# Optimization experiments

Hardware: AMD Instinct MI355X
Metric: run time of the kernel (lower is better)

Reference implementation:

```python
import jax, jax.numpy as jnp
import numpy as np

N_NODES = 50000
N_EDGES = 800000
IN_FEATS = 256
HIDDEN = 128
OUT_FEATS = 64


def setup_inputs() -> dict:
    key = jax.random.key(0)
    k1, k2, k3, k4, k5 = jax.random.split(key, 5)
    x = jax.random.normal(k1, (N_NODES, IN_FEATS), dtype=jnp.float32)
    src = jax.random.randint(k2, (N_EDGES,), 0, N_NODES, dtype=jnp.int64)
    dst = jax.random.randint(k3, (N_EDGES,), 0, N_NODES, dtype=jnp.int64)
    # Glorot-ish init for linear weights (DGL GraphConv uses xavier_uniform)
    W1 = jax.random.normal(k4, (IN_FEATS, HIDDEN), dtype=jnp.float32) / np.sqrt(IN_FEATS)
    W2 = jax.random.normal(k5, (HIDDEN, OUT_FEATS), dtype=jnp.float32) / np.sqrt(HIDDEN)
    b1 = jnp.zeros((HIDDEN,), dtype=jnp.float32)
    b2 = jnp.zeros((OUT_FEATS,), dtype=jnp.float32)
    return {"x": x, "src": src, "dst": dst, "W1": W1, "b1": b1, "W2": W2, "b2": b2}


def _norms(src, dst, n_nodes):
    ones = jnp.ones(src.shape[0], dtype=jnp.float32)
    deg_out = jax.ops.segment_sum(ones, src, num_segments=n_nodes)
    deg_in = jax.ops.segment_sum(ones, dst, num_segments=n_nodes)
    # DGL clamps zero degrees to 1 to avoid inf
    norm_src = jnp.power(jnp.clip(deg_out, 1.0, None), -0.5)  # [N]
    norm_dst = jnp.power(jnp.clip(deg_in, 1.0, None), -0.5)   # [N]
    return norm_src, norm_dst


def _gcn_layer(h, W, b, src, dst, norm_src, norm_dst, n_nodes):
    # norm='both': D_dst^{-1/2} A D_src^{-1/2} (h W) + b
    # multiply by W first (in_feats >= out_feats -> cheaper aggregation)
    m = (h * norm_src[:, None]) @ W            # [N, out]
    agg = jax.ops.segment_sum(m[src], dst, num_segments=n_nodes)  # [N, out]
    return agg * norm_dst[:, None] + b


def reference(x, src, dst, W1, b1, W2, b2):
    n = x.shape[0]
    norm_src, norm_dst = _norms(src, dst, n)
    h = _gcn_layer(x, W1, b1, src, dst, norm_src, norm_dst, n)
    h = jax.nn.relu(h)
    h = _gcn_layer(h, W2, b2, src, dst, norm_src, norm_dst, n)
    return h
```

## Files before the change

### kernel.cpp

```cpp
#include <hip/hip_runtime.h>

#define N_NODES 50000
#define N_EDGES 800000
#define IN_FEATS 256
#define HIDDEN 128
#define OUT_FEATS 64

#define NCHUNK 64
#define EPC 12500
#define NBH 16384
#define NRH 4
#define NBTH (NRH * NBH)
#define HBLKH (NRH * NCHUNK)
#define NBF 8192
#define NRF 7
#define FBLK (NRF * NCHUNK)
#define ROWBLK ((N_NODES + 63) / 64)

typedef _Float16 f16;
typedef _Float16 f16x8 __attribute__((ext_vector_type(8)));
typedef float f32x4 __attribute__((ext_vector_type(4)));

__global__ __launch_bounds__(256) void wtrans(const float* __restrict__ W1,
                                              const float* __restrict__ W2,
                                              f16* __restrict__ W1T,
                                              f16* __restrict__ W2T) {
  int i = blockIdx.x * 256 + threadIdx.x;
  if (i < 128 * 256) {
    int n = i >> 8, k = i & 255;
    W1T[i] = (f16)W1[k * 128 + n];
  } else {
    int j = i - 128 * 256;
    int n = j >> 7, k = j & 127;
    W2T[j] = (f16)W2[k * 64 + n];
  }
}

__global__ __launch_bounds__(256) void hist_gemm_kernel(
    const int* __restrict__ src, const int* __restrict__ dst,
    unsigned* __restrict__ hist_src, unsigned* __restrict__ hist_dst,
    const f16* __restrict__ W1T, const float* __restrict__ x,
    f16* __restrict__ m1) {
  __shared__ __align__(16) unsigned smem[8192];
  if (blockIdx.x < HBLKH) {
    unsigned* ls = smem;
    unsigned* ld2 = smem + NBH / 4;
    const int r = blockIdx.x % NRH;
    const int c = blockIdx.x / NRH;
    const int lo = r * NBH;
    for (int i = threadIdx.x; i < NBH / 4; i += 256) {
      ls[i] = 0;
      ld2[i] = 0;
    }
    __syncthreads();
    const int4* s4 = (const int4*)(src + c * EPC);
    const int4* d4 = (const int4*)(dst + c * EPC);
    for (int i = threadIdx.x; i < EPC / 4; i += 256) {
      int4 s = s4[i];
      int4 d = d4[i];
      unsigned b;
      b = (unsigned)(s.x - lo); if (b < NBH) atomicAdd(&ls[b >> 2], 1u << ((b & 3) << 3));
      b = (unsigned)(s.y - lo); if (b < NBH) atomicAdd(&ls[b >> 2], 1u << ((b & 3) << 3));
      b = (unsigned)(s.z - lo); if (b < NBH) atomicAdd(&ls[b >> 2], 1u << ((b & 3) << 3));
      b = (unsigned)(s.w - lo); if (b < NBH) atomicAdd(&ls[b >> 2], 1u << ((b & 3) << 3));
      b = (unsigned)(d.x - lo); if (b < NBH) atomicAdd(&ld2[b >> 2], 1u << ((b & 3) << 3));
      b = (unsigned)(d.y - lo); if (b < NBH) atomicAdd(&ld2[b >> 2], 1u << ((b & 3) << 3));
      b = (unsigned)(d.z - lo); if (b < NBH) atomicAdd(&ld2[b >> 2], 1u << ((b & 3) << 3));
      b = (unsigned)(d.w - lo); if (b < NBH) atomicAdd(&ld2[b >> 2], 1u << ((b & 3) << 3));
    }
    __syncthreads();
    unsigned* hs = hist_src + ((long)c * NBTH + lo) / 4;
    unsigned* hd = hist_dst + ((long)c * NBTH + lo) / 4;
    for (int i = threadIdx.x; i < NBH / 4; i += 256) {
      hs[i] = ls[i];
      hd[i] = ld2[i];
    }
  } else {
    char* BsBytes = (char*)smem;
    const int rb = blockIdx.x - HBLKH;
    const int wave = threadIdx.x >> 6;
    const int lane = threadIdx.x & 63;
    const int m = lane & 15;
    const int q = lane >> 4;
    const int row0 = rb * 64 + wave * 16;
    const int ra = min(row0 + m, N_NODES - 1);

    f16x8 a[8];
#pragma unroll
    for (int ki = 0; ki < 8; ++ki) {
      const float* p = x + (long)ra * IN_FEATS + ki * 32 + q * 8;
      float4 u0 = *(const float4*)p;
      float4 u1 = *(const float4*)(p + 4);
      a[ki][0] = (f16)u0.x; a[ki][1] = (f16)u0.y;
      a[ki][2] = (f16)u0.z; a[ki][3] = (f16)u0.w;
      a[ki][4] = (f16)u1.x; a[ki][5] = (f16)u1.y;
      a[ki][6] = (f16)u1.z; a[ki][7] = (f16)u1.w;
    }

    for (int h = 0; h < 2; ++h) {
      const int col0 = h * 64;
#pragma unroll
      for (int idx = threadIdx.x; idx < 64 * 32; idx += 256) {
        int n = idx >> 5;
        int kq = idx & 31;
        f16x8 v = *(const f16x8*)(W1T + (col0 + n) * IN_FEATS + kq * 8);
        unsigned bo = (unsigned)(n * 512 + kq * 16);
        bo ^= (unsigned)((n & 7) << 4);
        *(f16x8*)(BsBytes + bo) = v;
      }
      __syncthreads();

      f32x4 acc[4];
#pragma unroll
      for (int t = 0; t < 4; ++t) acc[t] = (f32x4){0.f, 0.f, 0.f, 0.f};

#pragma unroll
      for (int ki = 0; ki < 8; ++ki) {
        const int kb2 = (ki * 32 + q * 8) * 2;
#pragma unroll
        for (int t = 0; t < 4; ++t) {
          int nrow = t * 16 + m;
          unsigned bo = (unsigned)(nrow * 512 + kb2);
          bo ^= (unsigned)((nrow & 7) << 4);
          f16x8 bfr = *(const f16x8*)(BsBytes + bo);
          acc[t] = __builtin_amdgcn_mfma_f32_16x16x32_f16(a[ki], bfr, acc[t], 0, 0, 0);
        }
      }
      __syncthreads();

#pragma unroll
      for (int rr = 0; rr < 4; ++rr) {
        int row = row0 + q * 4 + rr;
        if (row < N_NODES) {
#pragma unroll
          for (int t = 0; t < 4; ++t)
            m1[(long)row * HIDDEN + col0 + t * 16 + m] = (f16)acc[t][rr];
        }
      }
    }
  }
}

__global__ __launch_bounds__(256) void reduce_kernel(
    const unsigned* __restrict__ hist_src, unsigned* __restrict__ hist_dst,
    int* __restrict__ deg_in, float* __restrict__ norm_src,
    float* __restrict__ norm_dst, int* __restrict__ partial) {
  const unsigned char* hs = (const unsigned char*)hist_src;
  unsigned char* hd = (unsigned char*)hist_dst;
  int n = blockIdx.x * 256 + threadIdx.x;
  int run = 0;
  if (n < N_NODES) {
    int so = 0;
#pragma unroll 8
    for (int c = 0; c < NCHUNK; ++c) so += hs[(long)c * NBTH + n];
    norm_src[n] = rsqrtf((float)max(so, 1));
#pragma unroll 8
    for (int c = 0; c < NCHUNK; ++c) {
      int t = hd[(long)c * NBTH + n];
      hd[(long)c * NBTH + n] = (unsigned char)run;
      run += t;
    }
    deg_in[n] = run;
    norm_dst[n] = rsqrtf((float)max(run, 1));
  }
  __shared__ int sd[256];
  sd[threadIdx.x] = run;
  __syncthreads();
  for (int s = 128; s > 0; s >>= 1) {
    if (threadIdx.x < s) sd[threadIdx.x] += sd[threadIdx.x + s];
    __syncthreads();
  }
  if (threadIdx.x == 0) partial[blockIdx.x] = sd[0];
}

__global__ __launch_bounds__(256) void scan3(const int* __restrict__ deg,
                                             const int* __restrict__ partial,
                                             int* __restrict__ rowptr) {
  __shared__ int sd[256];
  __shared__ int sp[256];
  const int w = blockIdx.x;
  int pv = (threadIdx.x < 196) ? partial[threadIdx.x] : 0;
  sp[threadIdx.x] = pv;
  __syncthreads();
  for (int off = 1; off < 256; off <<= 1) {
    int t = sp[threadIdx.x] +
            ((threadIdx.x >= off) ? sp[threadIdx.x - off] : 0);
    __syncthreads();
    sp[threadIdx.x] = t;
    __syncthreads();
  }
  const int base = (w == 0) ? 0 : sp[w - 1];
  int i = w * 256 + threadIdx.x;
  int v = (i < N_NODES) ? deg[i] : 0;
  sd[threadIdx.x] = v;
  __syncthreads();
  for (int off = 1; off < 256; off <<= 1) {
    int t = sd[threadIdx.x] +
            ((threadIdx.x >= off) ? sd[threadIdx.x - off] : 0);
    __syncthreads();
    sd[threadIdx.x] = t;
    __syncthreads();
  }
  if (i < N_NODES) rowptr[i] = base + sd[threadIdx.x] - v;
  if (w == 0 && threadIdx.x == 0) rowptr[N_NODES] = N_EDGES;
}

__global__ __launch_bounds__(256) void fill_csr(
    const int* __restrict__ src, const int* __restrict__ dst,
    const int* __restrict__ rowptr, const unsigned* __restrict__ pref32,
    int* __restrict__ col) {
  __shared__ int cur[NBF];
  const unsigned char* pref = (const unsigned char*)pref32;
  const int r = blockIdx.x % NRF;
  const int c = blockIdx.x / NRF;
  const int lo = r * NBF;
  for (int i = threadIdx.x; i < NBF; i += 256) {
    int n = lo + i;
    cur[i] = (n < N_NODES) ? rowptr[n] + pref[(long)c * NBTH + n] : 0;
  }
  __syncthreads();
  const int4* s4 = (const int4*)(src + c * EPC);
  const int4* d4 = (const int4*)(dst + c * EPC);
  for (int i = threadIdx.x; i < EPC / 4; i += 256) {
    int4 s = s4[i];
    int4 d = d4[i];
    unsigned b;
    b = (unsigned)(d.x - lo);
    if (b < NBF) col[atomicAdd(&cur[b], 1)] = s.x;
    b = (unsigned)(d.y - lo);
    if (b < NBF) col[atomicAdd(&cur[b], 1)] = s.y;
    b = (unsigned)(d.z - lo);
    if (b < NBF) col[atomicAdd(&cur[b], 1)] = s.z;
    b = (unsigned)(d.w - lo);
    if (b < NBF) col[atomicAdd(&cur[b], 1)] = s.w;
  }
}

template <int K, int NC, int TN, bool FP32IN>
__global__ __launch_bounds__(256) void gemm_mfma(
    const void* __restrict__ Xv, const f16* __restrict__ WT,
    const float* __restrict__ ns, f16* __restrict__ Mout) {
  constexpr int KI = K / 32;
  constexpr int COLBLK = NC / (TN * 16);
  constexpr int KP = K + 8;
  __shared__ f16 Bs[TN * 16 * KP];

  const int cb = blockIdx.x % COLBLK;
  const int rb = blockIdx.x / COLBLK;
  const int col0 = cb * TN * 16;
  const int wave = threadIdx.x >> 6;
  const int lane = threadIdx.x & 63;
  const int m = lane & 15;
  const int q = lane >> 4;
  const int row0 = rb * 64 + wave * 16;

  for (int idx = threadIdx.x; idx < TN * 16 * (K / 8); idx += 256) {
    int n = idx / (K / 8);
    int kk = idx % (K / 8);
    *(f16x8*)(Bs + n * KP + kk * 8) =
        *(const f16x8*)(WT + (long)(col0 + n) * K + kk * 8);
  }
  __syncthreads();

  const int ra = min(row0 + m, N_NODES - 1);
  const float s = FP32IN ? ns[ra] : 0.f;

  f32x4 acc[TN];
#pragma unroll
  for (int t = 0; t < TN; ++t) acc[t] = (f32x4){0.f, 0.f, 0.f, 0.f};

#pragma unroll
  for (int ki = 0; ki < KI; ++ki) {
    const int kb = ki * 32 + q * 8;
    f16x8 a;
    if (FP32IN) {
      const float* X = (const float*)Xv;
      const float* p = X + (long)ra * K + kb;
      float4 u0 = *(const float4*)p;
      float4 u1 = *(const float4*)(p + 4);
      a[0] = (f16)(u0.x * s); a[1] = (f16)(u0.y * s);
      a[2] = (f16)(u0.z * s); a[3] = (f16)(u0.w * s);
      a[4] = (f16)(u1.x * s); a[5] = (f16)(u1.y * s);
      a[6] = (f16)(u1.z * s); a[7] = (f16)(u1.w * s);
    } else {
      const f16* X = (const f16*)Xv;
      a = *(const f16x8*)(X + (long)ra * K + kb);
    }
#pragma unroll
    for (int t = 0; t < TN; ++t) {
      f16x8 b = *(const f16x8*)(Bs + (t * 16 + m) * KP + kb);
      acc[t] = __builtin_amdgcn_mfma_f32_16x16x32_f16(a, b, acc[t], 0, 0, 0);
    }
  }

#pragma unroll
  for (int r = 0; r < 4; ++r) {
    int row = row0 + q * 4 + r;
    if (row < N_NODES) {
#pragma unroll
      for (int t = 0; t < TN; ++t)
        Mout[(long)row * NC + col0 + t * 16 + m] = (f16)acc[t][r];
    }
  }
}

__global__ __launch_bounds__(256) void gather1_kernel(
    const f16* __restrict__ M, const int* __restrict__ rowptr,
    const int* __restrict__ col, const float* __restrict__ nd,
    const float* __restrict__ ns, const float* __restrict__ b,
    f16* __restrict__ out) {
  constexpr int LPR = 16;
  constexpr int EPW = 64 / LPR;
  const int wave = threadIdx.x >> 6;
  const int lane = threadIdx.x & 63;
  const int eg = lane / LPR;
  const int t = lane % LPR;
  const int n = blockIdx.x * 4 + wave;
  if (n >= N_NODES) return;
  const int beg = rowptr[n];
  const int end = rowptr[n + 1];

  float acc[8];
#pragma unroll
  for (int j = 0; j < 8; ++j) acc[j] = 0.f;

  int i = beg + eg;
  for (; i + EPW < end; i += 2 * EPW) {
    int s0 = col[i];
    int s1 = col[i + EPW];
    float n0 = ns[s0];
    float n1 = ns[s1];
    f16x8 v0 = *(const f16x8*)(M + (long)s0 * HIDDEN + t * 8);
    f16x8 v1 = *(const f16x8*)(M + (long)s1 * HIDDEN + t * 8);
#pragma unroll
    for (int j = 0; j < 8; ++j)
      acc[j] += n0 * (float)v0[j] + n1 * (float)v1[j];
  }
  if (i < end) {
    int s0 = col[i];
    float n0 = ns[s0];
    f16x8 v0 = *(const f16x8*)(M + (long)s0 * HIDDEN + t * 8);
#pragma unroll
    for (int j = 0; j < 8; ++j) acc[j] += n0 * (float)v0[j];
  }

#pragma unroll
  for (int m2 = LPR; m2 < 64; m2 <<= 1)
#pragma unroll
    for (int j = 0; j < 8; ++j) acc[j] += __shfl_xor(acc[j], m2, 64);

  if (eg == 0) {
    float s = nd[n];
    float sn = ns[n];
    float4 bb0 = *(const float4*)(b + t * 8);
    float4 bb1 = *(const float4*)(b + t * 8 + 4);
    f16x8 o;
    o[0] = (f16)(fmaxf(acc[0] * s + bb0.x, 0.f) * sn);
    o[1] = (f16)(fmaxf(acc[1] * s + bb0.y, 0.f) * sn);
    o[2] = (f16)(fmaxf(acc[2] * s + bb0.z, 0.f) * sn);
    o[3] = (f16)(fmaxf(acc[3] * s + bb0.w, 0.f) * sn);
    o[4] = (f16)(fmaxf(acc[4] * s + bb1.x, 0.f) * sn);
    o[5] = (f16)(fmaxf(acc[5] * s + bb1.y, 0.f) * sn);
    o[6] = (f16)(fmaxf(acc[6] * s + bb1.z, 0.f) * sn);
    o[7] = (f16)(fmaxf(acc[7] * s + bb1.w, 0.f) * sn);
    *(f16x8*)(out + (long)n * HIDDEN + t * 8) = o;
  }
}

__global__ __launch_bounds__(256) void gather2_kernel(
    const f16* __restrict__ M, const int* __restrict__ rowptr,
    const int* __restrict__ col, const float* __restrict__ nd,
    const float* __restrict__ b, float* __restrict__ out) {
  constexpr int LPR = 8;
  constexpr int EPW = 64 / LPR;
  const int wave = threadIdx.x >> 6;
  const int lane = threadIdx.x & 63;
  const int eg = lane / LPR;
  const int t = lane % LPR;
  const int n = blockIdx.x * 4 + wave;
  if (n >= N_NODES) return;
  const int beg = rowptr[n];
  const int end = rowptr[n + 1];

  float acc[8];
#pragma unroll
  for (int j = 0; j < 8; ++j) acc[j] = 0.f;

  int i = beg + eg;
  for (; i + EPW < end; i += 2 * EPW) {
    int s0 = col[i];
    int s1 = col[i + EPW];
    f16x8 v0 = *(const f16x8*)(M + (long)s0 * OUT_FEATS + t * 8);
    f16x8 v1 = *(const f16x8*)(M + (long)s1 * OUT_FEATS + t * 8);
#pragma unroll
    for (int j = 0; j < 8; ++j) acc[j] += (float)v0[j] + (float)v1[j];
  }
  if (i < end) {
    int s0 = col[i];
    f16x8 v0 = *(const f16x8*)(M + (long)s0 * OUT_FEATS + t * 8);
#pragma unroll
    for (int j = 0; j < 8; ++j) acc[j] += (float)v0[j];
  }

#pragma unroll
  for (int m2 = LPR; m2 < 64; m2 <<= 1)
#pragma unroll
    for (int j = 0; j < 8; ++j) acc[j] += __shfl_xor(acc[j], m2, 64);

  if (eg == 0) {
    float s = nd[n];
    float4 bb0 = *(const float4*)(b + t * 8);
    float4 bb1 = *(const float4*)(b + t * 8 + 4);
    float4 o0, o1;
    o0.x = acc[0] * s + bb0.x;
    o0.y = acc[1] * s + bb0.y;
    o0.z = acc[2] * s + bb0.z;
    o0.w = acc[3] * s + bb0.w;
    o1.x = acc[4] * s + bb1.x;
    o1.y = acc[5] * s + bb1.y;
    o1.z = acc[6] * s + bb1.z;
    o1.w = acc[7] * s + bb1.w;
    *(float4*)(out + (long)n * OUT_FEATS + t * 8) = o0;
    *(float4*)(out + (long)n * OUT_FEATS + t * 8 + 4) = o1;
  }
}

extern "C" void kernel_launch(void* const* d_in, const int* in_sizes, int n_in,
                              void* d_out, int out_size, void* d_ws,
                              size_t ws_size, hipStream_t stream) {
  const float* x = (const float*)d_in[0];
  const int* src = (const int*)d_in[1];
  const int* dst = (const int*)d_in[2];
  const float* W1 = (const float*)d_in[3];
  const float* b1 = (const float*)d_in[4];
  const float* W2 = (const float*)d_in[5];
  const float* b2 = (const float*)d_in[6];
  float* out = (float*)d_out;

  int* wi = (int*)d_ws;
  int* partial = wi;
  int* rowptr = wi + 256;
  int* deg_in = wi + 50260;
  int* col = wi + 100260;
  float* wf = (float*)d_ws + 900260;
  float* norm_src = wf;
  float* norm_dst = wf + 50000;
  f16* fh = (f16*)(wf + 100000);
  f16* W1T = fh;
  f16* W2T = fh + 128 * 256;
  f16* m1 = W2T + 64 * 128;
  f16* h1p = m1 + (long)50048 * 128;
  f16* m2 = h1p + (long)50048 * 128;

  unsigned* hist_src = (unsigned*)h1p;
  unsigned* hist_dst = hist_src + (long)NCHUNK * NBTH / 4;

  const int nb_nodes = (N_NODES + 255) / 256;

  wtrans<<<160, 256, 0, stream>>>(W1, W2, W1T, W2T);
  hist_gemm_kernel<<<HBLKH + ROWBLK, 256, 0, stream>>>(
      src, dst, hist_src, hist_dst, W1T, x, m1);
  reduce_kernel<<<nb_nodes, 256, 0, stream>>>(hist_src, hist_dst, deg_in,
                                              norm_src, norm_dst, partial);
  scan3<<<nb_nodes, 256, 0, stream>>>(deg_in, partial, rowptr);
  fill_csr<<<FBLK, 256, 0, stream>>>(src, dst, rowptr, hist_dst, col);

  gather1_kernel<<<(N_NODES + 3) / 4, 256, 0, stream>>>(m1, rowptr, col,
                                                        norm_dst, norm_src, b1,
                                                        h1p);

  gemm_mfma<HIDDEN, OUT_FEATS, 4, false>
      <<<ROWBLK, 256, 0, stream>>>(h1p, W2T, norm_src, m2);
  gather2_kernel<<<(N_NODES + 3) / 4, 256, 0, stream>>>(m2, rowptr, col,
                                                        norm_dst, b2, out);
}
```

Before: 221.6 us.

## Fuse layer-1 gather with layer-2 GEMM via shared-memory row tile

Layer-1 aggregation and the second GEMM now run in one kernel. Each 256-thread block aggregates 16 nodes into a shared-memory tile, then multiplies that tile by W2T with one 16x16x32 MFMA per wave per k-step and writes m2 directly. This removes the h1p round trip through global memory and one kernel launch. In exchange each wave processes 4 nodes serially, so there are fewer blocks to hide gather latency, and W2T is read straight from global by every block.

```diff
diff --git a/kernel.cpp b/kernel.cpp
--- a/kernel.cpp
+++ b/kernel.cpp
@@ -236,134 +236,88 @@
   }
 }
 
-template <int K, int NC, int TN, bool FP32IN>
-__global__ __launch_bounds__(256) void gemm_mfma(
-    const void* __restrict__ Xv, const f16* __restrict__ WT,
-    const float* __restrict__ ns, f16* __restrict__ Mout) {
-  constexpr int KI = K / 32;
-  constexpr int COLBLK = NC / (TN * 16);
-  constexpr int KP = K + 8;
-  __shared__ f16 Bs[TN * 16 * KP];
-
-  const int cb = blockIdx.x % COLBLK;
-  const int rb = blockIdx.x / COLBLK;
-  const int col0 = cb * TN * 16;
-  const int wave = threadIdx.x >> 6;
-  const int lane = threadIdx.x & 63;
-  const int m = lane & 15;
-  const int q = lane >> 4;
-  const int row0 = rb * 64 + wave * 16;
-
-  for (int idx = threadIdx.x; idx < TN * 16 * (K / 8); idx += 256) {
-    int n = idx / (K / 8);
-    int kk = idx % (K / 8);
-    *(f16x8*)(Bs + n * KP + kk * 8) =
-        *(const f16x8*)(WT + (long)(col0 + n) * K + kk * 8);
-  }
-  __syncthreads();
-
-  const int ra = min(row0 + m, N_NODES - 1);
-  const float s = FP32IN ? ns[ra] : 0.f;
-
-  f32x4 acc[TN];
-#pragma unroll
-  for (int t = 0; t < TN; ++t) acc[t] = (f32x4){0.f, 0.f, 0.f, 0.f};
-
-#pragma unroll
-  for (int ki = 0; ki < KI; ++ki) {
-    const int kb = ki * 32 + q * 8;
-    f16x8 a;
-    if (FP32IN) {
-      const float* X = (const float*)Xv;
-      const float* p = X + (long)ra * K + kb;
-      float4 u0 = *(const float4*)p;
-      float4 u1 = *(const float4*)(p + 4);
-      a[0] = (f16)(u0.x * s); a[1] = (f16)(u0.y * s);
-      a[2] = (f16)(u0.z * s); a[3] = (f16)(u0.w * s);
-      a[4] = (f16)(u1.x * s); a[5] = (f16)(u1.y * s);
-      a[6] = (f16)(u1.z * s); a[7] = (f16)(u1.w * s);
-    } else {
-      const f16* X = (const f16*)Xv;
-      a = *(const f16x8*)(X + (long)ra * K + kb);
-    }
-#pragma unroll
-    for (int t = 0; t < TN; ++t) {
-      f16x8 b = *(const f16x8*)(Bs + (t * 16 + m) * KP + kb);
-      acc[t] = __builtin_amdgcn_mfma_f32_16x16x32_f16(a, b, acc[t], 0, 0, 0);
-    }
-  }
-
-#pragma unroll
-  for (int r = 0; r < 4; ++r) {
-    int row = row0 + q * 4 + r;
-    if (row < N_NODES) {
-#pragma unroll
-      for (int t = 0; t < TN; ++t)
-        Mout[(long)row * NC + col0 + t * 16 + m] = (f16)acc[t][r];
-    }
-  }
-}
-
-__global__ __launch_bounds__(256) void gather1_kernel(
+__global__ __launch_bounds__(256) void gather_gemm2_kernel(
     const f16* __restrict__ M, const int* __restrict__ rowptr,
     const int* __restrict__ col, const float* __restrict__ nd,
     const float* __restrict__ ns, const float* __restrict__ b,
-    f16* __restrict__ out) {
+    const f16* __restrict__ W2T, f16* __restrict__ m2) {
   constexpr int LPR = 16;
   constexpr int EPW = 64 / LPR;
+  constexpr int RS = 136;
+  __shared__ __align__(16) f16 rows[16 * RS];
   const int wave = threadIdx.x >> 6;
   const int lane = threadIdx.x & 63;
   const int eg = lane / LPR;
   const int t = lane % LPR;
-  const int n = blockIdx.x * 4 + wave;
-  if (n >= N_NODES) return;
-  const int beg = rowptr[n];
-  const int end = rowptr[n + 1];
-
-  float acc[8];
-#pragma unroll
-  for (int j = 0; j < 8; ++j) acc[j] = 0.f;
-
-  int i = beg + eg;
-  for (; i + EPW < end; i += 2 * EPW) {
-    int s0 = col[i];
-    int s1 = col[i + EPW];
-    float n0 = ns[s0];
-    float n1 = ns[s1];
-    f16x8 v0 = *(const f16x8*)(M + (long)s0 * HIDDEN + t * 8);
-    f16x8 v1 = *(const f16x8*)(M + (long)s1 * HIDDEN + t * 8);
-#pragma unroll
-    for (int j = 0; j < 8; ++j)
-      acc[j] += n0 * (float)v0[j] + n1 * (float)v1[j];
-  }
-  if (i < end) {
-    int s0 = col[i];
-    float n0 = ns[s0];
-    f16x8 v0 = *(const f16x8*)(M + (long)s0 * HIDDEN + t * 8);
-#pragma unroll
-    for (int j = 0; j < 8; ++j) acc[j] += n0 * (float)v0[j];
-  }
-
-#pragma unroll
-  for (int m2 = LPR; m2 < 64; m2 <<= 1)
-#pragma unroll
-    for (int j = 0; j < 8; ++j) acc[j] += __shfl_xor(acc[j], m2, 64);
-
-  if (eg == 0) {
-    float s = nd[n];
-    float sn = ns[n];
-    float4 bb0 = *(const float4*)(b + t * 8);
-    float4 bb1 = *(const float4*)(b + t * 8 + 4);
-    f16x8 o;
-    o[0] = (f16)(fmaxf(acc[0] * s + bb0.x, 0.f) * sn);
-    o[1] = (f16)(fmaxf(acc[1] * s + bb0.y, 0.f) * sn);
-    o[2] = (f16)(fmaxf(acc[2] * s + bb0.z, 0.f) * sn);
-    o[3] = (f16)(fmaxf(acc[3] * s + bb0.w, 0.f) * sn);
-    o[4] = (f16)(fmaxf(acc[4] * s + bb1.x, 0.f) * sn);
-    o[5] = (f16)(fmaxf(acc[5] * s + bb1.y, 0.f) * sn);
-    o[6] = (f16)(fmaxf(acc[6] * s + bb1.z, 0.f) * sn);
-    o[7] = (f16)(fmaxf(acc[7] * s + bb1.w, 0.f) * sn);
-    *(f16x8*)(out + (long)n * HIDDEN + t * 8) = o;
+  const int base = blockIdx.x * 16;
+
+  for (int s = 0; s < 4; ++s) {
+    const int n = base + wave * 4 + s;
+    const int beg = rowptr[n];
+    const int end = rowptr[n + 1];
+
+    float acc[8];
+#pragma unroll
+    for (int j = 0; j < 8; ++j) acc[j] = 0.f;
+
+    int i = beg + eg;
+    for (; i + EPW < end; i += 2 * EPW) {
+      int s0 = col[i];
+      int s1 = col[i + EPW];
+      float n0 = ns[s0];
+      float n1 = ns[s1];
+      f16x8 v0 = *(const f16x8*)(M + (long)s0 * HIDDEN + t * 8);
+      f16x8 v1 = *(const f16x8*)(M + (long)s1 * HIDDEN + t * 8);
+#pragma unroll
+      for (int j = 0; j < 8; ++j)
+        acc[j] += n0 * (float)v0[j] + n1 * (float)v1[j];
+    }
+    if (i < end) {
+      int s0 = col[i];
+      float n0 = ns[s0];
+      f16x8 v0 = *(const f16x8*)(M + (long)s0 * HIDDEN + t * 8);
+#pragma unroll
+      for (int j = 0; j < 8; ++j) acc[j] += n0 * (float)v0[j];
+    }
+
+#pragma unroll
+    for (int mm = LPR; mm < 64; mm <<= 1)
+#pragma unroll
+      for (int j = 0; j < 8; ++j) acc[j] += __shfl_xor(acc[j], mm, 64);
+
+    if (eg == 0) {
+      float sc = nd[n];
+      float sn = ns[n];
+      float4 bb0 = *(const float4*)(b + t * 8);
+      float4 bb1 = *(const float4*)(b + t * 8 + 4);
+      f16x8 o;
+      o[0] = (f16)(fmaxf(acc[0] * sc + bb0.x, 0.f) * sn);
+      o[1] = (f16)(fmaxf(acc[1] * sc + bb0.y, 0.f) * sn);
+      o[2] = (f16)(fmaxf(acc[2] * sc + bb0.z, 0.f) * sn);
+      o[3] = (f16)(fmaxf(acc[3] * sc + bb0.w, 0.f) * sn);
+      o[4] = (f16)(fmaxf(acc[4] * sc + bb1.x, 0.f) * sn);
+      o[5] = (f16)(fmaxf(acc[5] * sc + bb1.y, 0.f) * sn);
+      o[6] = (f16)(fmaxf(acc[6] * sc + bb1.z, 0.f) * sn);
+      o[7] = (f16)(fmaxf(acc[7] * sc + bb1.w, 0.f) * sn);
+      *(f16x8*)(rows + (wave * 4 + s) * RS + t * 8) = o;
+    }
+  }
+  __syncthreads();
+
+  const int m = lane & 15;
+  const int q = lane >> 4;
+  f32x4 acc2 = (f32x4){0.f, 0.f, 0.f, 0.f};
+#pragma unroll
+  for (int ki = 0; ki < 4; ++ki) {
+    f16x8 a = *(const f16x8*)(rows + m * RS + ki * 32 + q * 8);
+    f16x8 bf =
+        *(const f16x8*)(W2T + (wave * 16 + m) * HIDDEN + ki * 32 + q * 8);
+    acc2 = __builtin_amdgcn_mfma_f32_16x16x32_f16(a, bf, acc2, 0, 0, 0);
+  }
+#pragma unroll
+  for (int r = 0; r < 4; ++r) {
+    int row = base + q * 4 + r;
+    m2[(long)row * OUT_FEATS + wave * 16 + m] = (f16)acc2[r];
   }
 }
 
@@ -403,9 +357,9 @@
   }
 
 #pragma unroll
-  for (int m2 = LPR; m2 < 64; m2 <<= 1)
-#pragma unroll
-    for (int j = 0; j < 8; ++j) acc[j] += __shfl_xor(acc[j], m2, 64);
+  for (int m2v = LPR; m2v < 64; m2v <<= 1)
+#pragma unroll
+    for (int j = 0; j < 8; ++j) acc[j] += __shfl_xor(acc[j], m2v, 64);
 
   if (eg == 0) {
     float s = nd[n];
@@ -449,10 +403,10 @@
   f16* W1T = fh;
   f16* W2T = fh + 128 * 256;
   f16* m1 = W2T + 64 * 128;
-  f16* h1p = m1 + (long)50048 * 128;
-  f16* m2 = h1p + (long)50048 * 128;
-
-  unsigned* hist_src = (unsigned*)h1p;
+  f16* histbuf = m1 + (long)50048 * 128;
+  f16* m2 = histbuf + (long)50048 * 128;
+
+  unsigned* hist_src = (unsigned*)histbuf;
   unsigned* hist_dst = hist_src + (long)NCHUNK * NBTH / 4;
 
   const int nb_nodes = (N_NODES + 255) / 256;
@@ -465,12 +419,9 @@
   scan3<<<nb_nodes, 256, 0, stream>>>(deg_in, partial, rowptr);
   fill_csr<<<FBLK, 256, 0, stream>>>(src, dst, rowptr, hist_dst, col);
 
-  gather1_kernel<<<(N_NODES + 3) / 4, 256, 0, stream>>>(m1, rowptr, col,
-                                                        norm_dst, norm_src, b1,
-                                                        h1p);
-
-  gemm_mfma<HIDDEN, OUT_FEATS, 4, false>
-      <<<ROWBLK, 256, 0, stream>>>(h1p, W2T, norm_src, m2);
+  gather_gemm2_kernel<<<N_NODES / 16, 256, 0, stream>>>(
+      m1, rowptr, col, norm_dst, norm_src, b1, W2T, m2);
+
   gather2_kernel<<<(N_NODES + 3) / 4, 256, 0, stream>>>(m2, rowptr, col,
                                                         norm_dst, b2, out);
 }
```

New measurement: 216.6 us. 1.02x faster.
